# Optimization experiments

Measured on AMD Instinct MI355X. Metric: run time of the kernel, lower is better.

## Reference

```python
import jax, jax.numpy as jnp
import numpy as np

# Module hyperparameters (init_kwargs)
N_CODES = 1024    # context_size
Q_LEN = 8         # query_len
D_MODEL = 256     # d_model
BATCH = 16384
DECAY = 0.99
EPSILON = 1e-05


def setup_inputs() -> dict:
    key = jax.random.key(0)
    k1, k2, k3 = jax.random.split(key, 3)
    q = jax.random.normal(k1, (BATCH, Q_LEN, D_MODEL), jnp.float32)
    context = jax.random.normal(k2, (N_CODES, Q_LEN, D_MODEL), jnp.float32)
    ema_count = jnp.ones((N_CODES,), jnp.float32)
    ema_dw = jax.random.normal(k3, (N_CODES, Q_LEN, D_MODEL), jnp.float32) * 0.1
    return {"q": q, "context": context, "ema_count": ema_count, "ema_dw": ema_dw}


def _forward(q, context, ema_count, ema_dw):
    B, Q, D = q.shape
    N = context.shape[0]
    q_flat = q.reshape(B, Q * D)              # [B, QD]
    g_flat = context.reshape(N, Q * D)        # [N, QD]
    Dflat = Q * D

    # squared-euclidean cdist via the matmul expansion, then nearest code
    distances = (jnp.sum(q_flat * q_flat, axis=1, keepdims=True)
                 + jnp.sum(g_flat * g_flat, axis=1)
                 - 2.0 * (q_flat @ g_flat.T))                      # [B, N]
    indices = jnp.argmin(distances, axis=-1)                       # [B]

    # einsum('bn,nqd->bqd', one_hot, context) == gather
    q_context = context[indices]                                   # [B, Q, D]
    # einsum('bn,bqd->nqd', one_hot, q) == scatter-add by code id
    q_hat = jax.ops.segment_sum(q, indices, num_segments=N)        # [N, Q, D]

    # per-sample mean MSE (q_context detached in original)
    qld = jnp.mean((jax.lax.stop_gradient(q_context) - q) ** 2, axis=(1, 2))  # [B]

    # EMA codebook update (training mode, no-grad in original)
    counts = jax.ops.segment_sum(jnp.ones((B,), q.dtype), indices, num_segments=N)  # [N]
    ec = DECAY * ema_count + (1.0 - DECAY) * counts
    n = jnp.sum(ec)
    ec = (ec + EPSILON) / (n + Dflat * EPSILON) * n                # Laplace smoothing
    edw = DECAY * ema_dw + (1.0 - DECAY) * jax.lax.stop_gradient(q_hat)
    context_new = edw / ec[:, None, None]                          # [N, Q, D]

    # straight-through output uses the UPDATED (detached) context
    out_context = (q_hat + jax.lax.stop_gradient(context_new - q_hat)).reshape(-1, D)  # [N*Q, D]
    return qld, out_context, ec, edw, context_new


def reference(q, context, ema_count, ema_dw):
    return _forward(q, context, ema_count, ema_dw)
```

## Files before the change

kernel.cpp:

```cpp
#include <hip/hip_runtime.h>
#include <hip/hip_bf16.h>
#include <float.h>

#define BSZ 16384
#define NCODES 1024
#define QD 2048
#define NCHUNK 64
#define NCOLG 16

typedef _Float16 f16x8 __attribute__((ext_vector_type(8)));
typedef _Float16 f16x4 __attribute__((ext_vector_type(4)));
typedef float f32x4 __attribute__((ext_vector_type(4)));

static __device__ __forceinline__ float one_minus_decay() { return (float)(1.0 - 0.99); }

static __device__ __forceinline__ void async_copy16(const void* src, void* lds) {
    __builtin_amdgcn_global_load_lds((const __attribute__((address_space(1))) void*)src,
                                     (__attribute__((address_space(3))) void*)lds, 16, 0, 0);
}

__global__ void k_prep_all(const float* __restrict__ ctx, const float* __restrict__ q,
                           _Float16* __restrict__ gh, float* __restrict__ gsq,
                           _Float16* __restrict__ qh, float* __restrict__ qsq) {
    __shared__ float red[4];
    int tid = threadIdx.x;
    const float* src; _Float16* dh; float* nrm;
    if (blockIdx.x < NCODES) {
        size_t n = blockIdx.x;
        src = ctx + n * QD; dh = gh + n * QD; nrm = gsq + n;
    } else {
        size_t b = blockIdx.x - NCODES;
        src = q + b * QD; dh = qh + b * QD; nrm = qsq + b;
    }
    int c = tid * 8;
    float4 t0 = *(const float4*)(src + c);
    float4 t1 = *(const float4*)(src + c + 4);
    float s = t0.x * t0.x + t0.y * t0.y + t0.z * t0.z + t0.w * t0.w
            + t1.x * t1.x + t1.y * t1.y + t1.z * t1.z + t1.w * t1.w;
    f16x8 h;
    h[0] = (_Float16)t0.x; h[1] = (_Float16)t0.y;
    h[2] = (_Float16)t0.z; h[3] = (_Float16)t0.w;
    h[4] = (_Float16)t1.x; h[5] = (_Float16)t1.y;
    h[6] = (_Float16)t1.z; h[7] = (_Float16)t1.w;
    *(f16x8*)(dh + c) = h;
    for (int off = 32; off > 0; off >>= 1) s += __shfl_down(s, off);
    if ((tid & 63) == 0) red[tid >> 6] = s;
    __syncthreads();
    if (tid == 0) *nrm = red[0] + red[1] + red[2] + red[3];
}

__global__ void k_prep_r17(const float* __restrict__ ctx, const float* __restrict__ q,
                           _Float16* __restrict__ gh, float* __restrict__ gsq,
                           float* __restrict__ qsq) {
    int tid = threadIdx.x;
    if (blockIdx.x < NCODES) {
        __shared__ float red[4];
        int n = blockIdx.x;
        float s = 0.f;
#pragma unroll
        for (int i = 0; i < 2; ++i) {
            int c = (tid + i * 256) * 4;
            float4 t = *(const float4*)(ctx + (size_t)n * QD + c);
            f16x4 h;
            h[0] = (_Float16)t.x; h[1] = (_Float16)t.y;
            h[2] = (_Float16)t.z; h[3] = (_Float16)t.w;
            *(f16x4*)(gh + (size_t)n * QD + c) = h;
            s += t.x * t.x + t.y * t.y + t.z * t.z + t.w * t.w;
        }
        for (int off = 32; off > 0; off >>= 1) s += __shfl_down(s, off);
        if ((tid & 63) == 0) red[tid >> 6] = s;
        __syncthreads();
        if (tid == 0) gsq[n] = red[0] + red[1] + red[2] + red[3];
    } else {
        int w = tid >> 6, lane = tid & 63;
        int b = (blockIdx.x - NCODES) * 4 + w;
        const float4* row = (const float4*)(q + (size_t)b * QD);
        float s = 0.f;
#pragma unroll
        for (int i = 0; i < 8; ++i) {
            float4 v = row[lane + i * 64];
            s += v.x * v.x + v.y * v.y + v.z * v.z + v.w * v.w;
        }
        for (int off = 32; off > 0; off >>= 1) s += __shfl_down(s, off);
        if (lane == 0) qsq[b] = s;
    }
}

__launch_bounds__(256)
__global__ void k_dist_pre(const _Float16* __restrict__ qh, const _Float16* __restrict__ gh,
                           const float* __restrict__ gsq,
                           float* __restrict__ pval, int* __restrict__ pidx) {
    __shared__ _Float16 ah[2][128][64];
    __shared__ _Float16 bh[2][128][64];

    const int tid = threadIdx.x;
    const int lane = tid & 63, wid = tid >> 6;
    const int wr = wid >> 1, wc = wid & 1;
    const int n0 = blockIdx.x;
    const int xcd = n0 & 7, j = n0 >> 3;
    const int col = j & 7, rowt = xcd * 16 + (j >> 3);
    const int colBase = col * 128, rowBase = rowt * 128;
    const int fr = lane & 15, kg = lane >> 4;

    const int srow = lane >> 3;
    const int gran = (lane & 7) ^ (lane >> 3);

    f32x4 acc[4][4];
#pragma unroll
    for (int m = 0; m < 4; ++m)
#pragma unroll
        for (int n = 0; n < 4; ++n) acc[m][n] = (f32x4)0.f;

#define STAGE_TILE(KB, BUF)                                                           \
    {                                                                                 \
        _Pragma("unroll")                                                             \
        for (int i_ = 0; i_ < 4; ++i_) {                                              \
            int g_ = wid * 4 + i_;                                                    \
            size_t ro_ = (size_t)(rowBase + g_ * 8 + srow) * QD + (KB) + gran * 8;    \
            size_t co_ = (size_t)(colBase + g_ * 8 + srow) * QD + (KB) + gran * 8;    \
            async_copy16(qh + ro_, &ah[BUF][g_ * 8][0]);                              \
            async_copy16(gh + co_, &bh[BUF][g_ * 8][0]);                              \
        }                                                                             \
    }

#define COMPUTE_TILE(BUF)                                                             \
    {                                                                                 \
        const char* ahB_ = (const char*)&ah[BUF][0][0];                               \
        const char* bhB_ = (const char*)&bh[BUF][0][0];                               \
        _Pragma("unroll")                                                             \
        for (int h_ = 0; h_ < 2; ++h_) {                                              \
            f16x8 a_h[4], b_h[4];                                                     \
            _Pragma("unroll")                                                         \
            for (int m_ = 0; m_ < 4; ++m_) {                                          \
                int ar_ = wr * 64 + m_ * 16 + fr;                                     \
                int off_ = ar_ * 128 + ((h_ * 64 + kg * 16) ^ ((ar_ & 7) << 4));      \
                a_h[m_] = *(const f16x8*)(ahB_ + off_);                               \
            }                                                                         \
            _Pragma("unroll")                                                         \
            for (int n_ = 0; n_ < 4; ++n_) {                                          \
                int br_ = wc * 64 + n_ * 16 + fr;                                     \
                int off_ = br_ * 128 + ((h_ * 64 + kg * 16) ^ ((br_ & 7) << 4));      \
                b_h[n_] = *(const f16x8*)(bhB_ + off_);                               \
            }                                                                         \
            _Pragma("unroll")                                                         \
            for (int m_ = 0; m_ < 4; ++m_)                                            \
                _Pragma("unroll")                                                     \
                for (int n_ = 0; n_ < 4; ++n_)                                        \
                    acc[m_][n_] = __builtin_amdgcn_mfma_f32_16x16x32_f16(             \
                        a_h[m_], b_h[n_], acc[m_][n_], 0, 0, 0);                      \
        }                                                                             \
    }

    STAGE_TILE(0, 0);
    STAGE_TILE(64, 1);

    for (int t = 0; t < 31; ++t) {
        asm volatile("s_waitcnt vmcnt(8)" ::: "memory");
        __builtin_amdgcn_s_barrier();
        COMPUTE_TILE(t & 1);
        __builtin_amdgcn_s_barrier();
        if (t < 30) STAGE_TILE((t + 2) * 64, t & 1);
    }
    asm volatile("s_waitcnt vmcnt(0)" ::: "memory");
    __builtin_amdgcn_s_barrier();
    COMPUTE_TILE(1);

#undef STAGE_TILE
#undef COMPUTE_TILE

    float mv[4][4]; int mi[4][4];
#pragma unroll
    for (int m = 0; m < 4; ++m)
#pragma unroll
        for (int r = 0; r < 4; ++r) { mv[m][r] = FLT_MAX; mi[m][r] = 0x7fffffff; }
#pragma unroll
    for (int n = 0; n < 4; ++n) {
        int c = colBase + wc * 64 + n * 16 + fr;
        float gq = gsq[c];
#pragma unroll
        for (int m = 0; m < 4; ++m)
#pragma unroll
            for (int r = 0; r < 4; ++r) {
                float d = gq - 2.0f * acc[m][n][r];
                if (d < mv[m][r]) { mv[m][r] = d; mi[m][r] = c; }
            }
    }
#pragma unroll
    for (int off = 1; off < 16; off <<= 1) {
#pragma unroll
        for (int m = 0; m < 4; ++m)
#pragma unroll
            for (int r = 0; r < 4; ++r) {
                float ov = __shfl_xor(mv[m][r], off);
                int   oi = __shfl_xor(mi[m][r], off);
                if (ov < mv[m][r] || (ov == mv[m][r] && oi < mi[m][r])) { mv[m][r] = ov; mi[m][r] = oi; }
            }
    }
    if (fr == 0) {
        const size_t slot = (size_t)(col * 2 + wc) * BSZ;
#pragma unroll
        for (int m = 0; m < 4; ++m)
#pragma unroll
            for (int r = 0; r < 4; ++r) {
                int grow = rowBase + wr * 64 + m * 16 + kg * 4 + r;
                pval[slot + grow] = mv[m][r];
                pidx[slot + grow] = mi[m][r];
            }
    }
}

__launch_bounds__(256)
__global__ void k_dist_r17(const float* __restrict__ q, const _Float16* __restrict__ gh,
                           const float* __restrict__ gsq,
                           float* __restrict__ pval, int* __restrict__ pidx) {
    __shared__ _Float16 ah[128][64];
    __shared__ _Float16 bh[128][64];

    const int tid = threadIdx.x;
    const int lane = tid & 63, wid = tid >> 6;
    const int wr = wid >> 1, wc = wid & 1;
    const int n0 = blockIdx.x;
    const int xcd = n0 & 7, j = n0 >> 3;
    const int col = j & 7, rowt = xcd * 16 + (j >> 3);
    const int colBase = col * 128, rowBase = rowt * 128;
    const int fr = lane & 15, kg = lane >> 4;

    char* ahB = (char*)&ah[0][0];
    const char* bhB = (const char*)&bh[0][0];

    f32x4 acc[4][4];
#pragma unroll
    for (int m = 0; m < 4; ++m)
#pragma unroll
        for (int n = 0; n < 4; ++n) acc[m][n] = (f32x4)0.f;

    for (int kb = 0; kb < QD; kb += 64) {
        __syncthreads();
#pragma unroll
        for (int s = 0; s < 8; ++s) {
            int f = s * 256 + tid;
            int row = f >> 4, k4 = (f & 15) * 4;
            float4 t = *(const float4*)(q + (size_t)(rowBase + row) * QD + kb + k4);
            f16x4 h;
            h[0] = (_Float16)t.x; h[1] = (_Float16)t.y;
            h[2] = (_Float16)t.z; h[3] = (_Float16)t.w;
            int byt = (row * 128 + k4 * 2) ^ ((row & 7) << 4);
            *(f16x4*)(ahB + byt) = h;
        }
#pragma unroll
        for (int i = 0; i < 4; ++i) {
            int g = wid * 4 + i;
            int row = g * 8 + (lane >> 3);
            int gran = (lane & 7) ^ (lane >> 3);
            size_t goff = (size_t)(colBase + row) * QD + kb + gran * 8;
            async_copy16(gh + goff, &bh[g * 8][0]);
        }
        __syncthreads();

#pragma unroll
        for (int h = 0; h < 2; ++h) {
            f16x8 a_h[4], b_h[4];
#pragma unroll
            for (int m = 0; m < 4; ++m) {
                int ar = wr * 64 + m * 16 + fr;
                int off = ar * 128 + ((h * 64 + kg * 16) ^ ((ar & 7) << 4));
                a_h[m] = *(const f16x8*)(ahB + off);
            }
#pragma unroll
            for (int n = 0; n < 4; ++n) {
                int br = wc * 64 + n * 16 + fr;
                int off = br * 128 + ((h * 64 + kg * 16) ^ ((br & 7) << 4));
                b_h[n] = *(const f16x8*)(bhB + off);
            }
#pragma unroll
            for (int m = 0; m < 4; ++m)
#pragma unroll
                for (int n = 0; n < 4; ++n)
                    acc[m][n] = __builtin_amdgcn_mfma_f32_16x16x32_f16(a_h[m], b_h[n], acc[m][n], 0, 0, 0);
        }
    }

    float mv[4][4]; int mi[4][4];
#pragma unroll
    for (int m = 0; m < 4; ++m)
#pragma unroll
        for (int r = 0; r < 4; ++r) { mv[m][r] = FLT_MAX; mi[m][r] = 0x7fffffff; }
#pragma unroll
    for (int n = 0; n < 4; ++n) {
        int c = colBase + wc * 64 + n * 16 + fr;
        float gq = gsq[c];
#pragma unroll
        for (int m = 0; m < 4; ++m)
#pragma unroll
            for (int r = 0; r < 4; ++r) {
                float d = gq - 2.0f * acc[m][n][r];
                if (d < mv[m][r]) { mv[m][r] = d; mi[m][r] = c; }
            }
    }
#pragma unroll
    for (int off = 1; off < 16; off <<= 1) {
#pragma unroll
        for (int m = 0; m < 4; ++m)
#pragma unroll
            for (int r = 0; r < 4; ++r) {
                float ov = __shfl_xor(mv[m][r], off);
                int   oi = __shfl_xor(mi[m][r], off);
                if (ov < mv[m][r] || (ov == mv[m][r] && oi < mi[m][r])) { mv[m][r] = ov; mi[m][r] = oi; }
            }
    }
    if (fr == 0) {
        const size_t slot = (size_t)(col * 2 + wc) * BSZ;
#pragma unroll
        for (int m = 0; m < 4; ++m)
#pragma unroll
            for (int r = 0; r < 4; ++r) {
                int grow = rowBase + wr * 64 + m * 16 + kg * 4 + r;
                pval[slot + grow] = mv[m][r];
                pidx[slot + grow] = mi[m][r];
            }
    }
}

__global__ void k_merge(const float* __restrict__ pval, const int* __restrict__ pidx,
                        const float* __restrict__ qsq,
                        int* __restrict__ idx_out, float* __restrict__ qld,
                        int* __restrict__ chunkhist) {
    __shared__ int h[NCODES];
    int c = blockIdx.x, tid = threadIdx.x;
    int b = c * 256 + tid;
#pragma unroll
    for (int s = 0; s < 4; ++s) h[tid + s * 256] = 0;
    float bv = pval[b]; int bi = pidx[b];
    for (int y = 1; y < NCOLG; ++y) {
        float v = pval[(size_t)y * BSZ + b]; int ii = pidx[(size_t)y * BSZ + b];
        if (v < bv || (v == bv && ii < bi)) { bv = v; bi = ii; }
    }
    idx_out[b] = bi;
    qld[b] = (qsq[b] + bv) * (1.0f / (float)QD);
    __syncthreads();
    atomicAdd(&h[bi], 1);
    __syncthreads();
#pragma unroll
    for (int s = 0; s < 4; ++s) chunkhist[c * NCODES + tid + s * 256] = h[tid + s * 256];
}

__global__ void k_scan(const int* __restrict__ chunkhist, int* __restrict__ base,
                       int* __restrict__ counts, int* __restrict__ offsets,
                       const float* __restrict__ ema_count, float* __restrict__ ec_out) {
    __shared__ int s[NCODES];
    __shared__ float e2[NCODES];
    int code = threadIdx.x;
    int run = 0;
    for (int c = 0; c < NCHUNK; ++c) {
        base[c * NCODES + code] = run;
        run += chunkhist[c * NCODES + code];
    }
    counts[code] = run;
    s[code] = run; __syncthreads();
    for (int off = 1; off < NCODES; off <<= 1) {
        int v = (code >= off) ? s[code - off] : 0;
        __syncthreads();
        s[code] += v; __syncthreads();
    }
    offsets[code] = s[code] - run;
    float er = 0.99f * ema_count[code] + one_minus_decay() * (float)run;
    e2[code] = er; __syncthreads();
    for (int off = 512; off > 0; off >>= 1) {
        if (code < off) e2[code] += e2[code + off];
        __syncthreads();
    }
    float n = e2[0];
    ec_out[code] = (er + 1e-5f) / (n + (float)(2048.0 * 1e-5)) * n;
}

__global__ void k_fill(const int* __restrict__ idx, const int* __restrict__ base,
                       const int* __restrict__ offsets, int* __restrict__ list) {
    __shared__ int sidx[256];
    int c = blockIdx.x, tid = threadIdx.x;
    int b = c * 256 + tid;
    int n = idx[b];
    sidx[tid] = n; __syncthreads();
    int rank = 0;
    for (int j = 0; j < tid; ++j) rank += (sidx[j] == n);
    list[offsets[n] + base[c * NCODES + n] + rank] = b;
}

__global__ void k_qhat_h(const _Float16* __restrict__ qh, const int* __restrict__ counts,
                         const int* __restrict__ offsets, const int* __restrict__ list,
                         float* __restrict__ qhat) {
    int n = blockIdx.x;
    int col = blockIdx.y * 256 + threadIdx.x;
    int cnt = counts[n];
    const int* lp = list + offsets[n];
    float a0 = 0.f, a1 = 0.f, a2 = 0.f, a3 = 0.f, a4 = 0.f, a5 = 0.f, a6 = 0.f, a7 = 0.f;
    int i = 0;
    for (; i + 8 <= cnt; i += 8) {
        int b0 = lp[i], b1 = lp[i + 1], b2 = lp[i + 2], b3 = lp[i + 3];
        int b4 = lp[i + 4], b5 = lp[i + 5], b6 = lp[i + 6], b7 = lp[i + 7];
        a0 += (float)qh[(size_t)b0 * QD + col]; a1 += (float)qh[(size_t)b1 * QD + col];
        a2 += (float)qh[(size_t)b2 * QD + col]; a3 += (float)qh[(size_t)b3 * QD + col];
        a4 += (float)qh[(size_t)b4 * QD + col]; a5 += (float)qh[(size_t)b5 * QD + col];
        a6 += (float)qh[(size_t)b6 * QD + col]; a7 += (float)qh[(size_t)b7 * QD + col];
    }
    for (; i < cnt; ++i) a0 += (float)qh[(size_t)lp[i] * QD + col];
    float r = ((a0 + a1) + (a2 + a3)) + ((a4 + a5) + (a6 + a7));
    qhat[(size_t)n * QD + col] = r;
}

__global__ void k_qhat_f(const float* __restrict__ q, const int* __restrict__ counts,
                         const int* __restrict__ offsets, const int* __restrict__ list,
                         float* __restrict__ qhat) {
    int n = blockIdx.x;
    int col = blockIdx.y * 256 + threadIdx.x;
    int cnt = counts[n];
    const int* lp = list + offsets[n];
    float a0 = 0.f, a1 = 0.f, a2 = 0.f, a3 = 0.f, a4 = 0.f, a5 = 0.f, a6 = 0.f, a7 = 0.f;
    int i = 0;
    for (; i + 8 <= cnt; i += 8) {
        int b0 = lp[i], b1 = lp[i + 1], b2 = lp[i + 2], b3 = lp[i + 3];
        int b4 = lp[i + 4], b5 = lp[i + 5], b6 = lp[i + 6], b7 = lp[i + 7];
        a0 += q[(size_t)b0 * QD + col]; a1 += q[(size_t)b1 * QD + col];
        a2 += q[(size_t)b2 * QD + col]; a3 += q[(size_t)b3 * QD + col];
        a4 += q[(size_t)b4 * QD + col]; a5 += q[(size_t)b5 * QD + col];
        a6 += q[(size_t)b6 * QD + col]; a7 += q[(size_t)b7 * QD + col];
    }
    for (; i < cnt; ++i) a0 += q[(size_t)lp[i] * QD + col];
    float r = ((a0 + a1) + (a2 + a3)) + ((a4 + a5) + (a6 + a7));
    qhat[(size_t)n * QD + col] = r;
}

__global__ void k_fin(const float* __restrict__ ema_dw, const float* __restrict__ ec,
                      const float* qhat, float* edw_out, float* ctxnew_out,
                      float* outctx_out) {
    size_t i = ((size_t)blockIdx.x * 256 + threadIdx.x) * 8;
    int n = (int)(i >> 11);
    float e = ec[n];
    float om = one_minus_decay();
#pragma unroll
    for (int h = 0; h < 2; ++h) {
        float4 dw = *(const float4*)(ema_dw + i + h * 4);
        float4 qh = *(const float4*)(qhat + i + h * 4);
        float4 ed, cn;
        ed.x = 0.99f * dw.x + om * qh.x; ed.y = 0.99f * dw.y + om * qh.y;
        ed.z = 0.99f * dw.z + om * qh.z; ed.w = 0.99f * dw.w + om * qh.w;
        cn.x = ed.x / e; cn.y = ed.y / e; cn.z = ed.z / e; cn.w = ed.w / e;
        *(float4*)(edw_out + i + h * 4) = ed;
        *(float4*)(ctxnew_out + i + h * 4) = cn;
        *(float4*)(outctx_out + i + h * 4) = cn;
    }
}

extern "C" void kernel_launch(void* const* d_in, const int* in_sizes, int n_in,
                              void* d_out, int out_size, void* d_ws, size_t ws_size,
                              hipStream_t stream) {
    const float* q         = (const float*)d_in[0];
    const float* ctx       = (const float*)d_in[1];
    const float* ema_count = (const float*)d_in[2];
    const float* ema_dw    = (const float*)d_in[3];

    float* out = (float*)d_out;
    float* o_qld    = out;
    float* o_outctx = out + BSZ;
    float* o_ec     = o_outctx + (size_t)NCODES * QD;
    float* o_edw    = o_ec + NCODES;
    float* o_ctxnew = o_edw + (size_t)NCODES * QD;

    char* w = (char*)d_ws;
    float* ws_gsq   = (float*)w;
    int* ws_idx     = (int*)(w + 4096);
    int* ws_counts  = (int*)(w + 4096 + 65536);
    int* ws_offsets = ws_counts + NCODES;
    int* ws_list    = ws_offsets + NCODES;

    const size_t presplit_need = (size_t)1048576 + (size_t)BSZ * QD * sizeof(_Float16);
    const bool use_pre = (ws_size >= presplit_need);
    _Float16* qh = (_Float16*)(w + 1048576);

    _Float16* gh = (_Float16*)o_ctxnew;
    float* pval  = o_edw;
    int*   pidx  = (int*)(o_edw + (size_t)NCOLG * BSZ);
    float* qsq   = o_edw + (size_t)2 * NCOLG * BSZ;
    int* chunkhist = (int*)o_outctx;
    int* basep     = chunkhist + NCHUNK * NCODES;
    float* qhat    = o_outctx;

    if (use_pre) {
        k_prep_all<<<NCODES + BSZ, 256, 0, stream>>>(ctx, q, gh, ws_gsq, qh, qsq);
        k_dist_pre<<<1024, 256, 0, stream>>>(qh, gh, ws_gsq, pval, pidx);
    } else {
        k_prep_r17<<<NCODES + BSZ / 4, 256, 0, stream>>>(ctx, q, gh, ws_gsq, qsq);
        k_dist_r17<<<1024, 256, 0, stream>>>(q, gh, ws_gsq, pval, pidx);
    }
    k_merge <<<NCHUNK, 256, 0, stream>>>(pval, pidx, qsq, ws_idx, o_qld, chunkhist);
    k_scan  <<<1, 1024, 0, stream>>>(chunkhist, basep, ws_counts, ws_offsets, ema_count, o_ec);
    k_fill  <<<NCHUNK, 256, 0, stream>>>(ws_idx, basep, ws_offsets, ws_list);
    if (use_pre) {
        k_qhat_h<<<dim3(NCODES, 8), 256, 0, stream>>>(qh, ws_counts, ws_offsets, ws_list, qhat);
    } else {
        k_qhat_f<<<dim3(NCODES, 8), 256, 0, stream>>>(q, ws_counts, ws_offsets, ws_list, qhat);
    }
    k_fin   <<<NCODES * QD / 2048, 256, 0, stream>>>(ema_dw, o_ec, qhat,
                                                     o_edw, o_ctxnew, o_outctx);
}
```

Before: 199.7 us.

## Load query operand straight to registers and restage codebook tiles per step

The query (A) operand of the distance GEMM is no longer staged through LDS. Each wave now loads its A fragments directly from global memory into registers, using a two-set register double buffer (aP/aQ). The codebook (B) operand is still async-copied into LDS, but now two 64-wide k-slices per iteration, bracketed by full __syncthreads. This removes A's LDS traffic and halves LDS usage. In exchange, the previous cross-iteration B prefetch is dropped, so B global latency is exposed every iteration, and A rows are fetched redundantly by the two column waves.

```diff
diff --git a/kernel.cpp b/kernel.cpp
--- a/kernel.cpp
+++ b/kernel.cpp
@@ -90,7 +90,6 @@
 __global__ void k_dist_pre(const _Float16* __restrict__ qh, const _Float16* __restrict__ gh,
                            const float* __restrict__ gsq,
                            float* __restrict__ pval, int* __restrict__ pidx) {
-    __shared__ _Float16 ah[2][128][64];
     __shared__ _Float16 bh[2][128][64];
 
     const int tid = threadIdx.x;
@@ -105,37 +104,31 @@
     const int srow = lane >> 3;
     const int gran = (lane & 7) ^ (lane >> 3);
 
+    const _Float16* aBase = qh + (size_t)(rowBase + wr * 64 + fr) * QD + kg * 8;
+
     f32x4 acc[4][4];
 #pragma unroll
     for (int m = 0; m < 4; ++m)
 #pragma unroll
         for (int n = 0; n < 4; ++n) acc[m][n] = (f32x4)0.f;
 
-#define STAGE_TILE(KB, BUF)                                                           \
+    f16x8 aP[4][2], aQ[4][2];
+
+#define LOAD_A(DST, KB)                                                               \
     {                                                                                 \
         _Pragma("unroll")                                                             \
-        for (int i_ = 0; i_ < 4; ++i_) {                                              \
-            int g_ = wid * 4 + i_;                                                    \
-            size_t ro_ = (size_t)(rowBase + g_ * 8 + srow) * QD + (KB) + gran * 8;    \
-            size_t co_ = (size_t)(colBase + g_ * 8 + srow) * QD + (KB) + gran * 8;    \
-            async_copy16(qh + ro_, &ah[BUF][g_ * 8][0]);                              \
-            async_copy16(gh + co_, &bh[BUF][g_ * 8][0]);                              \
-        }                                                                             \
-    }
-
-#define COMPUTE_TILE(BUF)                                                             \
+        for (int m_ = 0; m_ < 4; ++m_)                                                \
+            _Pragma("unroll")                                                         \
+            for (int h_ = 0; h_ < 2; ++h_)                                            \
+                DST[m_][h_] = *(const f16x8*)(aBase + (size_t)(m_ * 16) * QD + (KB) + h_ * 32); \
+    }
+
+#define COMPUTE_TILE(AREG, BUF)                                                       \
     {                                                                                 \
-        const char* ahB_ = (const char*)&ah[BUF][0][0];                               \
         const char* bhB_ = (const char*)&bh[BUF][0][0];                               \
         _Pragma("unroll")                                                             \
         for (int h_ = 0; h_ < 2; ++h_) {                                              \
-            f16x8 a_h[4], b_h[4];                                                     \
-            _Pragma("unroll")                                                         \
-            for (int m_ = 0; m_ < 4; ++m_) {                                          \
-                int ar_ = wr * 64 + m_ * 16 + fr;                                     \
-                int off_ = ar_ * 128 + ((h_ * 64 + kg * 16) ^ ((ar_ & 7) << 4));      \
-                a_h[m_] = *(const f16x8*)(ahB_ + off_);                               \
-            }                                                                         \
+            f16x8 b_h[4];                                                             \
             _Pragma("unroll")                                                         \
             for (int n_ = 0; n_ < 4; ++n_) {                                          \
                 int br_ = wc * 64 + n_ * 16 + fr;                                     \
@@ -147,25 +140,32 @@
                 _Pragma("unroll")                                                     \
                 for (int n_ = 0; n_ < 4; ++n_)                                        \
                     acc[m_][n_] = __builtin_amdgcn_mfma_f32_16x16x32_f16(             \
-                        a_h[m_], b_h[n_], acc[m_][n_], 0, 0, 0);                      \
+                        AREG[m_][h_], b_h[n_], acc[m_][n_], 0, 0, 0);                 \
         }                                                                             \
     }
 
-    STAGE_TILE(0, 0);
-    STAGE_TILE(64, 1);
-
-    for (int t = 0; t < 31; ++t) {
-        asm volatile("s_waitcnt vmcnt(8)" ::: "memory");
-        __builtin_amdgcn_s_barrier();
-        COMPUTE_TILE(t & 1);
-        __builtin_amdgcn_s_barrier();
-        if (t < 30) STAGE_TILE((t + 2) * 64, t & 1);
-    }
-    asm volatile("s_waitcnt vmcnt(0)" ::: "memory");
-    __builtin_amdgcn_s_barrier();
-    COMPUTE_TILE(1);
-
-#undef STAGE_TILE
+    LOAD_A(aP, 0);
+
+    for (int kb = 0; kb < QD; kb += 128) {
+        __syncthreads();
+#pragma unroll
+        for (int d = 0; d < 2; ++d) {
+#pragma unroll
+            for (int i = 0; i < 4; ++i) {
+                int g = wid * 4 + i;
+                size_t co = (size_t)(colBase + g * 8 + srow) * QD + kb + d * 64 + gran * 8;
+                async_copy16(gh + co, &bh[d][g * 8][0]);
+            }
+        }
+        __syncthreads();
+
+        LOAD_A(aQ, kb + 64);
+        COMPUTE_TILE(aP, 0);
+        if (kb + 128 < QD) LOAD_A(aP, kb + 128);
+        COMPUTE_TILE(aQ, 1);
+    }
+
+#undef LOAD_A
 #undef COMPUTE_TILE
 
     float mv[4][4]; int mi[4][4];
```

New measurement: 278.5 us. +39.5%, slower.
